# Kernel optimization log

Measured on AMD Instinct MI355X. Metric: run time of the kernel, lower is better.

The kernel has to match this reference:

```python
import jax, jax.numpy as jnp
import numpy as np

N = 200000   # nodes
R = 4        # relations
E = 1000000  # edges per relation
B = 1024     # graphs in batch


def _graph_conv(h, s, d, ew, W, b):
    """DGL GraphConv, norm='both', optional edge_weight. h:[N,F_in] -> [N,F_out]."""
    n = h.shape[0]
    ones = jnp.ones(s.shape[0], dtype=h.dtype)
    out_deg = jnp.clip(jax.ops.segment_sum(ones, s, num_segments=n), 1.0)
    in_deg = jnp.clip(jax.ops.segment_sum(ones, d, num_segments=n), 1.0)
    hs = h * jax.lax.rsqrt(out_deg)[:, None]          # src-side norm
    m = hs[s]                                         # gather: [E, F_in]
    if ew is not None:
        m = m * ew[:, None]
    agg = jax.ops.segment_sum(m, d, num_segments=n)   # scatter-sum: [N, F_in]
    rst = agg * jax.lax.rsqrt(in_deg)[:, None]        # dst-side norm
    return rst @ W + b


def _hetero_layer(h, src, dst, ew, W, b):
    out = None
    for r in range(R):
        ewr = None if ew is None else ew[r]
        o = _graph_conv(h, src[r], dst[r], ewr, W[r], b[r])
        out = o if out is None else out + o
    return out


def setup_inputs() -> dict:
    key = jax.random.key(0)
    ks = jax.random.split(key, 10)
    feat = jax.random.normal(ks[0], (N, 2), dtype=jnp.float32)
    src = jax.random.randint(ks[1], (R, E), 0, N, dtype=jnp.int32)
    dst = jax.random.randint(ks[2], (R, E), 0, N, dtype=jnp.int32)
    ew = jax.random.uniform(ks[3], (R, E), dtype=jnp.float32)
    graph_ids = jnp.sort(jax.random.randint(ks[4], (N,), 0, B, dtype=jnp.int32))
    W1 = jax.random.normal(ks[5], (R, 2, 16), dtype=jnp.float32) * 0.5
    b1 = jnp.zeros((R, 16), dtype=jnp.float32)
    W2 = jax.random.normal(ks[6], (R, 16, 16), dtype=jnp.float32) * 0.25
    b2 = jnp.zeros((R, 16), dtype=jnp.float32)
    Wc = jax.random.normal(ks[7], (16, 2), dtype=jnp.float32) * 0.25
    bc = jnp.zeros((2,), dtype=jnp.float32)
    return {"feat": feat, "src": src, "dst": dst, "ew": ew,
            "graph_ids": graph_ids, "W1": W1, "b1": b1,
            "W2": W2, "b2": b2, "Wc": Wc, "bc": bc}


def reference(feat, src, dst, ew, graph_ids, W1, b1, W2, b2, Wc, bc):
    # layer 1: per-relation weighted GraphConv, summed over relations
    h = _hetero_layer(feat, src, dst, ew, W1, b1)
    h = jax.nn.relu(h)
    # layer 2: no edge weights (kwargs not forwarded in original code)
    h = _hetero_layer(h, src, dst, None, W2, b2)
    # mean_nodes per graph in the batch
    sums = jax.ops.segment_sum(h, graph_ids, num_segments=B)          # [B,16]
    cnts = jax.ops.segment_sum(jnp.ones((N,), h.dtype), graph_ids, num_segments=B)
    hg = sums / jnp.clip(cnts, 1.0)[:, None]
    return hg @ Wc + bc                                               # [B,2]
```

## Files before the change

### kernel.cpp

```cpp
#include <hip/hip_runtime.h>
#include <hip/hip_fp16.h>

#define NN 200000
#define RR 4
#define EE 1000000
#define BB 1024
#define RN (RR*NN)

#define BSH 7
#define BSZ 128
#define NB 1563
#define RK (RR*NB)
#define EPB 8192
#define SBT 1024
#define BPR ((EE + EPB - 1) / EPB)
#define GSLOTS 32
#define CAPB 1024

#define SRC_OF(u)  (((u) >> 7) & 0x3FFFF)
#define DL_OF(u)   ((int)((u) & 127))
#define DEG_OF(u)  ((u) >> 25)

#define OFF_POOL   0
#define OFF_CNT    (OFF_POOL + BB*16)
#define OFF_GCUR_S (OFF_CNT + BB)
#define OFF_GCUR_D (OFF_GCUR_S + RK)
#define ZERO_UNITS (OFF_GCUR_D + RK)
#define OFF_DEGB   ZERO_UNITS
#define OFF_INVI   (OFF_DEGB + RN/4)
#define OFF_RW16   (OFF_INVI + RN)
#define OFF_AGG1   (OFF_RW16 + RN/2)
#define OFF_H1H    (OFF_AGG1 + RN*2)
#define OFF_KW_    (OFF_H1H + NN*8)
#define OFF_KW     (OFF_KW_ + (OFF_KW_ & 1))


__global__ __launch_bounds__(SBT) void k_scat_src(const int* __restrict__ src,
                                                  int* __restrict__ gcur_s,
                                                  unsigned char* __restrict__ srcbin) {
  __shared__ int cnt[NB];
  __shared__ int base[NB];
  __shared__ int lcur[NB];
  int t = threadIdx.x, r = blockIdx.y, c0 = blockIdx.x * EPB;
  for (int i = t; i < NB; i += SBT) cnt[i] = 0;
  __syncthreads();
  for (int i = t; i < EPB; i += SBT) {
    int e = c0 + i;
    if (e < EE) atomicAdd(&cnt[src[r * EE + e] >> BSH], 1);
  }
  __syncthreads();
  for (int b = t; b < NB; b += SBT) {
    int v = cnt[b];
    base[b] = v ? atomicAdd(&gcur_s[r * NB + b], v) : 0;
    lcur[b] = 0;
  }
  __syncthreads();
  for (int i = t; i < EPB; i += SBT) {
    int e = c0 + i;
    if (e < EE) {
      int s = src[r * EE + e];
      int b = s >> BSH;
      int off = base[b] + atomicAdd(&lcur[b], 1);
      if (off < CAPB)
        srcbin[(size_t)(r * NB + b) * CAPB + off] = (unsigned char)(s & (BSZ - 1));
    }
  }
}

__global__ __launch_bounds__(128) void k_deg(const unsigned char* __restrict__ srcbin,
                                             const int* __restrict__ gcur_s,
                                             unsigned char* __restrict__ degb) {
  __shared__ int cnt[BSZ];
  int t = threadIdx.x, b = blockIdx.x, r = blockIdx.y;
  cnt[t] = 0;
  __syncthreads();
  int k = r * NB + b;
  size_t st = (size_t)k * CAPB;
  int m = min(gcur_s[k], CAPB);
  for (int e = t; e < m; e += 128) atomicAdd(&cnt[srcbin[st + e]], 1);
  __syncthreads();
  int n = (b << BSH) + t;
  if (n < NN) degb[r * NN + n] = (unsigned char)min(max(cnt[t], 1), 63);
}

__global__ __launch_bounds__(SBT) void k_scat_dst(const int* __restrict__ src,
                                                  const int* __restrict__ dst,
                                                  const float* __restrict__ ew,
                                                  const unsigned char* __restrict__ degb,
                                                  int* __restrict__ gcur_d,
                                                  long long* __restrict__ kw) {
  __shared__ int cnt[NB];
  __shared__ int base[NB];
  __shared__ int lcur[NB];
  int t = threadIdx.x, r = blockIdx.y, c0 = blockIdx.x * EPB;
  for (int i = t; i < NB; i += SBT) cnt[i] = 0;
  __syncthreads();
  for (int i = t; i < EPB; i += SBT) {
    int e = c0 + i;
    if (e < EE) atomicAdd(&cnt[dst[r * EE + e] >> BSH], 1);
  }
  __syncthreads();
  for (int b = t; b < NB; b += SBT) {
    int v = cnt[b];
    base[b] = v ? atomicAdd(&gcur_d[r * NB + b], v) : 0;
    lcur[b] = 0;
  }
  __syncthreads();
  for (int i = t; i < EPB; i += SBT) {
    int e = c0 + i;
    if (e < EE) {
      int idx = r * EE + e;
      int d = dst[idx], s = src[idx];
      int b = d >> BSH;
      int off = base[b] + atomicAdd(&lcur[b], 1);
      if (off < CAPB) {
        unsigned dg = degb[r * NN + s];
        float io = rsqrtf((float)dg);
        unsigned short w1h = __half_as_ushort(__float2half_rn(ew[idx] * io));
        unsigned low = (unsigned)(d & (BSZ - 1)) | ((unsigned)s << 7) | (dg << 25);
        kw[(size_t)(r * NB + b) * CAPB + off] =
            (long long)(((unsigned long long)w1h << 32) | low);
      }
    }
  }
}

__global__ __launch_bounds__(256) void k_l1a(long long* __restrict__ kw,
                                             const int* __restrict__ gcur_d,
                                             const float* __restrict__ feat,
                                             float* __restrict__ invi,
                                             unsigned short* __restrict__ rw16,
                                             float* __restrict__ agg1) {
  __shared__ long long bufraw[CAPB];
  __shared__ long long bufsort[CAPB];
  __shared__ int cnt[BSZ];
  __shared__ int scn[BSZ];
  __shared__ int cur[BSZ];
  __shared__ float la[BSZ * 3];
  int t = threadIdx.x, b = blockIdx.x, r = blockIdx.y;
  int n0 = b << BSH;
  int k = r * NB + b;
  size_t st = (size_t)k * CAPB;
  int m = min(gcur_d[k], CAPB);
  if (t < BSZ) { cnt[t] = 0; la[t * 3] = 0.f; la[t * 3 + 1] = 0.f; }
  for (int i = t; i < m; i += 256) bufraw[i] = kw[st + i];
  __syncthreads();
  for (int i = t; i < m; i += 256)
    atomicAdd(&cnt[DL_OF((unsigned)bufraw[i])], 1);
  __syncthreads();
  if (t < BSZ) scn[t] = cnt[t];
  __syncthreads();
  for (int off = 1; off < BSZ; off <<= 1) {
    int v = (t < BSZ && t >= off) ? scn[t - off] : 0;
    __syncthreads();
    if (t < BSZ) scn[t] += v;
    __syncthreads();
  }
  if (t < BSZ) {
    int excl = scn[t] - cnt[t];
    cur[t] = excl;
    int n = n0 + t;
    if (n < NN) {
      invi[r * NN + n] = rsqrtf((float)max(cnt[t], 1));
      rw16[r * NN + n] = (unsigned short)excl;
    }
  }
  __syncthreads();
  for (int i = t; i < m; i += 256) {
    long long kv = bufraw[i];
    bufsort[atomicAdd(&cur[DL_OF((unsigned)kv)], 1)] = kv;
  }
  __syncthreads();
  {
    unsigned* up = (unsigned*)kw + 2 * st + CAPB;
    for (int i = t; i < m; i += 256) up[i] = (unsigned)bufsort[i];
  }
  {
    int f = t & 1, grp = t >> 1;
    int seg = (m + BSZ - 1) >> 7;
    int e = grp * seg;
    int e1 = min(e + seg, m);
    float acc = 0.f;
    int dlprev = -1, dlfirst = -1;
    for (; e < e1; e++) {
      long long kv = bufsort[e];
      unsigned low = (unsigned)kv;
      int dl = DL_OF(low);
      int s = SRC_OF(low);
      float w = __half2float(__ushort_as_half((unsigned short)((unsigned long long)kv >> 32)));
      float fv = feat[s * 2 + f];
      if (dl != dlprev) {
        if (dlprev < 0) dlfirst = dl;
        else if (dlprev == dlfirst) atomicAdd(&la[dlprev * 3 + f], acc);
        else la[dlprev * 3 + f] = acc;
        acc = 0.f; dlprev = dl;
      }
      acc += fv * w;
    }
    if (dlprev >= 0) atomicAdd(&la[dlprev * 3 + f], acc);
  }
  __syncthreads();
  if (t < BSZ) {
    int n = n0 + t;
    if (n < NN)
      ((float2*)agg1)[r * NN + n] = make_float2(la[t * 3], la[t * 3 + 1]);
  }
}

__device__ __forceinline__ unsigned pack2h(float a, float b) {
  __half2 h = __floats2half2_rn(a, b);
  return *reinterpret_cast<unsigned*>(&h);
}

__global__ __launch_bounds__(256) void k_l1b(const float* __restrict__ agg1,
                                             const float* __restrict__ invi,
                                             const float* __restrict__ W1,
                                             const float* __restrict__ b1,
                                             __half* __restrict__ h1h) {
  __shared__ float sW[RR * 2 * 16];
  __shared__ float sb[16];
  int t = threadIdx.x, b = blockIdx.x;
  if (t < RR * 2 * 16) sW[t] = W1[t];
  if (t < 16) {
    float s = 0.f;
    for (int r = 0; r < RR; r++) s += b1[r * 16 + t];
    sb[t] = s;
  }
  __syncthreads();
  int n = b * 256 + t;
  if (n >= NN) return;
  float acc[16];
#pragma unroll
  for (int j = 0; j < 16; j++) acc[j] = sb[j];
#pragma unroll
  for (int r = 0; r < RR; r++) {
    float iv = invi[r * NN + n];
    float2 a = ((const float2*)agg1)[r * NN + n];
    float a0 = a.x * iv, a1 = a.y * iv;
#pragma unroll
    for (int j = 0; j < 16; j++)
      acc[j] += a0 * sW[(r * 2 + 0) * 16 + j] + a1 * sW[(r * 2 + 1) * 16 + j];
  }
#pragma unroll
  for (int j = 0; j < 16; j++) acc[j] = fmaxf(acc[j], 0.f);
  uint4 u0, u1;
  u0.x = pack2h(acc[0], acc[1]);  u0.y = pack2h(acc[2], acc[3]);
  u0.z = pack2h(acc[4], acc[5]);  u0.w = pack2h(acc[6], acc[7]);
  u1.x = pack2h(acc[8], acc[9]);  u1.y = pack2h(acc[10], acc[11]);
  u1.z = pack2h(acc[12], acc[13]); u1.w = pack2h(acc[14], acc[15]);
  uint4* o = (uint4*)(h1h + (size_t)n * 16);
  o[0] = u0; o[1] = u1;
}

__device__ __forceinline__ void acc8(float* acc, uint4 u, float w) {
  float2 p;
  p = __half22float2(*(__half2*)&u.x); acc[0] += p.x * w; acc[1] += p.y * w;
  p = __half22float2(*(__half2*)&u.y); acc[2] += p.x * w; acc[3] += p.y * w;
  p = __half22float2(*(__half2*)&u.z); acc[4] += p.x * w; acc[5] += p.y * w;
  p = __half22float2(*(__half2*)&u.w); acc[6] += p.x * w; acc[7] += p.y * w;
}

__global__ __launch_bounds__(256) void k_l2(const long long* __restrict__ kw,
                                            const int* __restrict__ gcur_d,
                                            const unsigned short* __restrict__ rw16,
                                            const __half* __restrict__ h1h,
                                            const float* __restrict__ invi,
                                            const float* __restrict__ W2,
                                            const int* __restrict__ gid,
                                            float* __restrict__ pool,
                                            float* __restrict__ cnt) {
  __shared__ float agg[BSZ * 17];
  __shared__ float sW[16 * 16];
  __shared__ int   sg[BSZ];
  __shared__ unsigned short srw[BSZ + 1];
  __shared__ float gslot[GSLOTS * 16];
  __shared__ int   cslot[GSLOTS];
  __shared__ int   present[GSLOTS];
  int t = threadIdx.x, b = blockIdx.x, r = blockIdx.y;
  int n0 = b << BSH;
  int k = r * NB + b;
  int m = min(gcur_d[k], CAPB);
  sW[t] = W2[r * 256 + t];
  if (t < GSLOTS) { cslot[t] = 0; present[t] = 0; }
  for (int i = t; i < GSLOTS * 16; i += 256) gslot[i] = 0.f;
  if (t < BSZ) {
    int n = n0 + t;
    srw[t] = (n < NN) ? rw16[r * NN + n] : (unsigned short)m;
  }
  if (t == BSZ) srw[BSZ] = (unsigned short)m;
  __syncthreads();
  const uint4* h4p = (const uint4*)h1h;
  const unsigned* rb = (const unsigned*)kw + 2 * (size_t)k * CAPB + CAPB;
  int f8 = t & 1, g = t >> 1;
  int e = srw[g], en = srw[g + 1];
  float acc[8];
#pragma unroll
  for (int j = 0; j < 8; j++) acc[j] = 0.f;
  for (; e + 3 < en; e += 4) {
    unsigned r0 = rb[e], r1 = rb[e + 1], r2 = rb[e + 2], r3 = rb[e + 3];
    uint4 u0 = h4p[(size_t)SRC_OF(r0) * 2 + f8];
    uint4 u1 = h4p[(size_t)SRC_OF(r1) * 2 + f8];
    uint4 u2 = h4p[(size_t)SRC_OF(r2) * 2 + f8];
    uint4 u3 = h4p[(size_t)SRC_OF(r3) * 2 + f8];
    acc8(acc, u0, rsqrtf((float)DEG_OF(r0)));
    acc8(acc, u1, rsqrtf((float)DEG_OF(r1)));
    acc8(acc, u2, rsqrtf((float)DEG_OF(r2)));
    acc8(acc, u3, rsqrtf((float)DEG_OF(r3)));
  }
  for (; e < en; e++) {
    unsigned rr = rb[e];
    uint4 u = h4p[(size_t)SRC_OF(rr) * 2 + f8];
    acc8(acc, u, rsqrtf((float)DEG_OF(rr)));
  }
#pragma unroll
  for (int j = 0; j < 8; j++) agg[g * 17 + 8 * f8 + j] = acc[j];
  __syncthreads();
  int n = n0 + t;
  int g0 = gid[n0];
  bool valid = (t < BSZ) && (n < NN);
  float out[16];
#pragma unroll
  for (int j = 0; j < 16; j++) out[j] = 0.f;
  if (valid) {
    float iv = invi[r * NN + n];
#pragma unroll
    for (int kk = 0; kk < 16; kk++) {
      float a = agg[t * 17 + kk] * iv;
#pragma unroll
      for (int j = 0; j < 16; j++) out[j] += a * sW[kk * 16 + j];
    }
  }
  __syncthreads();
  if (t < BSZ) {
    sg[t] = valid ? (gid[n] - g0) : -1;
#pragma unroll
    for (int j = 0; j < 16; j++) agg[t * 17 + j] = out[j];
  }
  __syncthreads();
  {
    int f = t & 15, i0 = t >> 4;
    for (int i = i0; i < BSZ; i += 16) {
      int gsN = sg[i];
      if (gsN < 0) continue;
      float v = agg[i * 17 + f];
      if (gsN < GSLOTS) {
        atomicAdd(&gslot[gsN * 16 + f], v);
        if (f == 0) {
          present[gsN] = 1;
          if (r == 0) atomicAdd(&cslot[gsN], 1);
        }
      } else {
        atomicAdd(&pool[(g0 + gsN) * 16 + f], v);
        if (f == 0 && r == 0) atomicAdd(&cnt[g0 + gsN], 1.0f);
      }
    }
  }
  __syncthreads();
  if (t < GSLOTS * 16) {
    int gsN = t >> 4, f = t & 15;
    if (present[gsN]) atomicAdd(&pool[(g0 + gsN) * 16 + f], gslot[t]);
  }
  if (r == 0 && t < GSLOTS && cslot[t] > 0)
    atomicAdd(&cnt[g0 + t], (float)cslot[t]);
}

__global__ __launch_bounds__(256) void k_final(const float* __restrict__ pool,
                                               const float* __restrict__ cnt,
                                               const float* __restrict__ b2,
                                               const float* __restrict__ Wc,
                                               const float* __restrict__ bc,
                                               float* __restrict__ out) {
  int b = blockIdx.x * 256 + threadIdx.x;
  if (b >= BB) return;
  float c = cnt[b];
  float inv = 1.0f / fmaxf(c, 1.0f);
  float o0 = bc[0], o1 = bc[1];
#pragma unroll
  for (int j = 0; j < 16; j++) {
    float sb = 0.f;
    for (int r = 0; r < RR; r++) sb += b2[r * 16 + j];
    float v = (pool[b * 16 + j] + c * sb) * inv;
    o0 += v * Wc[j * 2 + 0];
    o1 += v * Wc[j * 2 + 1];
  }
  out[b * 2 + 0] = o0;
  out[b * 2 + 1] = o1;
}

extern "C" void kernel_launch(void* const* d_in, const int* in_sizes, int n_in,
                              void* d_out, int out_size, void* d_ws, size_t ws_size,
                              hipStream_t stream) {
  const float* feat = (const float*)d_in[0];
  const int*   src  = (const int*)d_in[1];
  const int*   dst  = (const int*)d_in[2];
  const float* ew   = (const float*)d_in[3];
  const int*   gid  = (const int*)d_in[4];
  const float* W1   = (const float*)d_in[5];
  const float* b1   = (const float*)d_in[6];
  const float* W2   = (const float*)d_in[7];
  const float* b2   = (const float*)d_in[8];
  const float* Wc   = (const float*)d_in[9];
  const float* bc   = (const float*)d_in[10];

  char* ws = (char*)d_ws;
  float* pool   = (float*)(ws + (size_t)OFF_POOL   * 4);
  float* cnt    = (float*)(ws + (size_t)OFF_CNT    * 4);
  int*   gcur_s = (int*)  (ws + (size_t)OFF_GCUR_S * 4);
  int*   gcur_d = (int*)  (ws + (size_t)OFF_GCUR_D * 4);
  unsigned char*  degb = (unsigned char*) (ws + (size_t)OFF_DEGB * 4);
  float* invi   = (float*)(ws + (size_t)OFF_INVI   * 4);
  unsigned short* rw16 = (unsigned short*)(ws + (size_t)OFF_RW16 * 4);
  float* agg1   = (float*)(ws + (size_t)OFF_AGG1   * 4);
  __half* h1h   = (__half*)(ws + (size_t)OFF_H1H   * 4);
  long long* kw = (long long*)(ws + (size_t)OFF_KW * 4);

  hipMemsetAsync(d_ws, 0, (size_t)ZERO_UNITS * 4, stream);

  k_scat_src<<<dim3(BPR, RR), SBT, 0, stream>>>(src, gcur_s, (unsigned char*)kw);
  k_deg     <<<dim3(NB, RR), 128, 0, stream>>>((const unsigned char*)kw, gcur_s, degb);
  k_scat_dst<<<dim3(BPR, RR), SBT, 0, stream>>>(src, dst, ew, degb, gcur_d, kw);
  k_l1a     <<<dim3(NB, RR), 256, 0, stream>>>(kw, gcur_d, feat, invi, rw16, agg1);
  k_l1b     <<<(NN + 255) / 256, 256, 0, stream>>>(agg1, invi, W1, b1, h1h);
  k_l2      <<<dim3(NB, RR), 256, 0, stream>>>(kw, gcur_d, rw16, h1h, invi, W2, gid, pool, cnt);
  k_final   <<<(BB + 255) / 256, 256, 0, stream>>>(pool, cnt, b2, Wc, bc, (float*)d_out);
}
```

Baseline: 333.2 us.

## Fuse source and destination binning into one scatter pass, defer degree norm

Merges the separate source-binning and destination-binning kernels into one kernel that reads src/dst once and bins both in the same pass. The out-degree scaling and packing of the degree into the edge record is moved from the scatter into k_l1a, applied to the shared-memory copy after the bucket load. The source bins now live in the agg1 region instead of aliasing the kw buffer. This saves one pass over the edge arrays and one launch, at the cost of doubled shared-memory histograms, lower occupancy in the scatter kernel, and an extra random degb gather inside k_l1a.

```diff
diff --git a/kernel.cpp b/kernel.cpp
--- a/kernel.cpp
+++ b/kernel.cpp
@@ -35,34 +35,56 @@
 #define OFF_KW     (OFF_KW_ + (OFF_KW_ & 1))
 
 
-__global__ __launch_bounds__(SBT) void k_scat_src(const int* __restrict__ src,
-                                                  int* __restrict__ gcur_s,
-                                                  unsigned char* __restrict__ srcbin) {
-  __shared__ int cnt[NB];
-  __shared__ int base[NB];
-  __shared__ int lcur[NB];
+__global__ __launch_bounds__(SBT) void k_scat(const int* __restrict__ src,
+                                              const int* __restrict__ dst,
+                                              const float* __restrict__ ew,
+                                              int* __restrict__ gcur_s,
+                                              int* __restrict__ gcur_d,
+                                              unsigned char* __restrict__ srcbin,
+                                              long long* __restrict__ kw) {
+  __shared__ int cntS[NB];
+  __shared__ int baseS[NB];
+  __shared__ int lcurS[NB];
+  __shared__ int cntD[NB];
+  __shared__ int baseD[NB];
+  __shared__ int lcurD[NB];
   int t = threadIdx.x, r = blockIdx.y, c0 = blockIdx.x * EPB;
-  for (int i = t; i < NB; i += SBT) cnt[i] = 0;
-  __syncthreads();
-  for (int i = t; i < EPB; i += SBT) {
-    int e = c0 + i;
-    if (e < EE) atomicAdd(&cnt[src[r * EE + e] >> BSH], 1);
-  }
-  __syncthreads();
-  for (int b = t; b < NB; b += SBT) {
-    int v = cnt[b];
-    base[b] = v ? atomicAdd(&gcur_s[r * NB + b], v) : 0;
-    lcur[b] = 0;
-  }
+  for (int i = t; i < NB; i += SBT) { cntS[i] = 0; cntD[i] = 0; }
   __syncthreads();
   for (int i = t; i < EPB; i += SBT) {
     int e = c0 + i;
     if (e < EE) {
-      int s = src[r * EE + e];
-      int b = s >> BSH;
-      int off = base[b] + atomicAdd(&lcur[b], 1);
-      if (off < CAPB)
-        srcbin[(size_t)(r * NB + b) * CAPB + off] = (unsigned char)(s & (BSZ - 1));
+      atomicAdd(&cntS[src[r * EE + e] >> BSH], 1);
+      atomicAdd(&cntD[dst[r * EE + e] >> BSH], 1);
+    }
+  }
+  __syncthreads();
+  for (int b = t; b < NB; b += SBT) {
+    int v = cntS[b];
+    baseS[b] = v ? atomicAdd(&gcur_s[r * NB + b], v) : 0;
+    lcurS[b] = 0;
+    int w = cntD[b];
+    baseD[b] = w ? atomicAdd(&gcur_d[r * NB + b], w) : 0;
+    lcurD[b] = 0;
+  }
+  __syncthreads();
+  for (int i = t; i < EPB; i += SBT) {
+    int e = c0 + i;
+    if (e < EE) {
+      int idx = r * EE + e;
+      int s = src[idx], d = dst[idx];
+      int bs = s >> BSH;
+      int offs = baseS[bs] + atomicAdd(&lcurS[bs], 1);
+      if (offs < CAPB)
+        srcbin[(size_t)(r * NB + bs) * CAPB + offs] = (unsigned char)(s & (BSZ - 1));
+      int bd = d >> BSH;
+      int offd = baseD[bd] + atomicAdd(&lcurD[bd], 1);
+      if (offd < CAPB) {
+        unsigned short ewh = __half_as_ushort(__float2half_rn(ew[idx]));
+        unsigned low = (unsigned)(d & (BSZ - 1)) | ((unsigned)s << 7);
+        kw[(size_t)(r * NB + bd) * CAPB + offd] =
+            (long long)(((unsigned long long)ewh << 32) | low);
+      }
     }
   }
 }
@@ -83,50 +105,9 @@
   if (n < NN) degb[r * NN + n] = (unsigned char)min(max(cnt[t], 1), 63);
 }
 
-__global__ __launch_bounds__(SBT) void k_scat_dst(const int* __restrict__ src,
-                                                  const int* __restrict__ dst,
-                                                  const float* __restrict__ ew,
-                                                  const unsigned char* __restrict__ degb,
-                                                  int* __restrict__ gcur_d,
-                                                  long long* __restrict__ kw) {
-  __shared__ int cnt[NB];
-  __shared__ int base[NB];
-  __shared__ int lcur[NB];
-  int t = threadIdx.x, r = blockIdx.y, c0 = blockIdx.x * EPB;
-  for (int i = t; i < NB; i += SBT) cnt[i] = 0;
-  __syncthreads();
-  for (int i = t; i < EPB; i += SBT) {
-    int e = c0 + i;
-    if (e < EE) atomicAdd(&cnt[dst[r * EE + e] >> BSH], 1);
-  }
-  __syncthreads();
-  for (int b = t; b < NB; b += SBT) {
-    int v = cnt[b];
-    base[b] = v ? atomicAdd(&gcur_d[r * NB + b], v) : 0;
-    lcur[b] = 0;
-  }
-  __syncthreads();
-  for (int i = t; i < EPB; i += SBT) {
-    int e = c0 + i;
-    if (e < EE) {
-      int idx = r * EE + e;
-      int d = dst[idx], s = src[idx];
-      int b = d >> BSH;
-      int off = base[b] + atomicAdd(&lcur[b], 1);
-      if (off < CAPB) {
-        unsigned dg = degb[r * NN + s];
-        float io = rsqrtf((float)dg);
-        unsigned short w1h = __half_as_ushort(__float2half_rn(ew[idx] * io));
-        unsigned low = (unsigned)(d & (BSZ - 1)) | ((unsigned)s << 7) | (dg << 25);
-        kw[(size_t)(r * NB + b) * CAPB + off] =
-            (long long)(((unsigned long long)w1h << 32) | low);
-      }
-    }
-  }
-}
-
 __global__ __launch_bounds__(256) void k_l1a(long long* __restrict__ kw,
                                              const int* __restrict__ gcur_d,
+                                             const unsigned char* __restrict__ degb,
                                              const float* __restrict__ feat,
                                              float* __restrict__ invi,
                                              unsigned short* __restrict__ rw16,
@@ -164,6 +145,17 @@
       invi[r * NN + n] = rsqrtf((float)max(cnt[t], 1));
       rw16[r * NN + n] = (unsigned short)excl;
     }
+  }
+  __syncthreads();
+  for (int i = t; i < m; i += 256) {
+    long long kv = bufraw[i];
+    unsigned low = (unsigned)kv;
+    int s = SRC_OF(low);
+    unsigned dg = degb[r * NN + s];
+    float ewf = __half2float(__ushort_as_half((unsigned short)((unsigned long long)kv >> 32)));
+    unsigned short w1h = __half_as_ushort(__float2half_rn(ewf * rsqrtf((float)dg)));
+    bufraw[i] = (long long)(((unsigned long long)w1h << 32) |
+                            (unsigned long long)(low | (dg << 25)));
   }
   __syncthreads();
   for (int i = t; i < m; i += 256) {
@@ -411,16 +403,16 @@
   float* invi   = (float*)(ws + (size_t)OFF_INVI   * 4);
   unsigned short* rw16 = (unsigned short*)(ws + (size_t)OFF_RW16 * 4);
   float* agg1   = (float*)(ws + (size_t)OFF_AGG1   * 4);
+  unsigned char* srcbin = (unsigned char*)(ws + (size_t)OFF_AGG1 * 4);
   __half* h1h   = (__half*)(ws + (size_t)OFF_H1H   * 4);
   long long* kw = (long long*)(ws + (size_t)OFF_KW * 4);
 
   hipMemsetAsync(d_ws, 0, (size_t)ZERO_UNITS * 4, stream);
 
-  k_scat_src<<<dim3(BPR, RR), SBT, 0, stream>>>(src, gcur_s, (unsigned char*)kw);
-  k_deg     <<<dim3(NB, RR), 128, 0, stream>>>((const unsigned char*)kw, gcur_s, degb);
-  k_scat_dst<<<dim3(BPR, RR), SBT, 0, stream>>>(src, dst, ew, degb, gcur_d, kw);
-  k_l1a     <<<dim3(NB, RR), 256, 0, stream>>>(kw, gcur_d, feat, invi, rw16, agg1);
-  k_l1b     <<<(NN + 255) / 256, 256, 0, stream>>>(agg1, invi, W1, b1, h1h);
-  k_l2      <<<dim3(NB, RR), 256, 0, stream>>>(kw, gcur_d, rw16, h1h, invi, W2, gid, pool, cnt);
-  k_final   <<<(BB + 255) / 256, 256, 0, stream>>>(pool, cnt, b2, Wc, bc, (float*)d_out);
-}
+  k_scat  <<<dim3(BPR, RR), SBT, 0, stream>>>(src, dst, ew, gcur_s, gcur_d, srcbin, kw);
+  k_deg   <<<dim3(NB, RR), 128, 0, stream>>>(srcbin, gcur_s, degb);
+  k_l1a   <<<dim3(NB, RR), 256, 0, stream>>>(kw, gcur_d, degb, feat, invi, rw16, agg1);
+  k_l1b   <<<(NN + 255) / 256, 256, 0, stream>>>(agg1, invi, W1, b1, h1h);
+  k_l2    <<<dim3(NB, RR), 256, 0, stream>>>(kw, gcur_d, rw16, h1h, invi, W2, gid, pool, cnt);
+  k_final <<<(BB + 255) / 256, 256, 0, stream>>>(pool, cnt, b2, Wc, bc, (float*)d_out);
+}
```

New measurement: 345.2 us. 1.04x slower.
